# Optimization experiments

Measured on AMD Instinct MI355X. Metric: run time of the kernel, lower is better.

## Reference

```python
import jax, jax.numpy as jnp
import numpy as np

N_NODES = 100000


def gcn_conv(x, edge_index, W, b):
    """PyG GCNConv: symmetric normalization with added self-loops.
    x: [N, Fin], edge_index: [2, E], W: [Fin, Fout], b: [Fout]
    """
    n = x.shape[0]
    h = x @ W  # [N, Fout] dense transform first (standard GCNConv order)
    loops = jnp.arange(n, dtype=edge_index.dtype)
    src = jnp.concatenate([edge_index[0], loops])  # self-loops appended
    dst = jnp.concatenate([edge_index[1], loops])
    deg = jax.ops.segment_sum(jnp.ones_like(dst, dtype=h.dtype), dst, num_segments=n)
    dinv = jax.lax.rsqrt(deg)  # deg >= 1 thanks to self-loops
    norm = dinv[src] * dinv[dst]  # [E+N]
    msgs = h[src] * norm[:, None]  # gather + scale
    out = jax.ops.segment_sum(msgs, dst, num_segments=n)  # scatter-add
    return out + b


def setup_inputs() -> dict:
    key = jax.random.key(0)
    k = jax.random.split(key, 9)
    in_c, hid, out_c = 128, 128, 64
    n_edges = 1600000
    x = jax.random.normal(k[0], (N_NODES, in_c), dtype=jnp.float32)
    edge_index = jax.random.randint(k[1], (2, n_edges), 0, N_NODES, dtype=jnp.int64)
    def lin(kw, kb, fan_in, fan_out):
        bound = 1.0 / np.sqrt(fan_in)
        W = jax.random.uniform(kw, (fan_in, fan_out), jnp.float32, -bound, bound)
        b = jax.random.uniform(kb, (fan_out,), jnp.float32, -bound, bound)
        return W, b
    W1, b1 = lin(k[2], k[3], in_c, hid)
    W2, b2 = lin(k[4], k[5], hid, hid)
    Wf, bf = lin(k[6], k[7], hid, out_c)
    return {"x": x, "edge_index": edge_index, "W1": W1, "b1": b1,
            "W2": W2, "b2": b2, "Wf": Wf, "bf": bf}


def reference(x, edge_index, W1, b1, W2, b2, Wf, bf):
    h = jax.nn.relu(gcn_conv(x, edge_index, W1, b1))
    h = jax.nn.relu(gcn_conv(h, edge_index, W2, b2))
    return h @ Wf + bf
```

## Files before the change

kernel.cpp:

```cpp
#include <hip/hip_runtime.h>
#include <stdint.h>

typedef short short8 __attribute__((ext_vector_type(8)));
typedef float floatx4 __attribute__((ext_vector_type(4)));
typedef float f32x2 __attribute__((ext_vector_type(2)));

#define BK 256

static __device__ __forceinline__ float bflo(unsigned int u) {
    union { unsigned int i; float f; } v; v.i = u << 16; return v.f;
}
static __device__ __forceinline__ float bfhi(unsigned int u) {
    union { unsigned int i; float f; } v; v.i = u & 0xffff0000u; return v.f;
}
static __device__ __forceinline__ unsigned short f2bf(float f) {
    union { float f; unsigned int i; } v; v.f = f;
    unsigned int u = v.i;
    unsigned int r = u + 0x7fffu + ((u >> 16) & 1u);
    return (unsigned short)(r >> 16);
}
static __device__ __forceinline__ f32x2 unp2(unsigned int u) {
    union { unsigned int i; float f; } lo, hi;
    lo.i = u << 16; hi.i = u & 0xffff0000u;
    f32x2 r; r.x = lo.f; r.y = hi.f; return r;
}


__global__ void k_wconv_all(const float* __restrict__ W1, const float* __restrict__ W2,
                            const float* __restrict__ Wf, unsigned short* __restrict__ wb1,
                            unsigned short* __restrict__ wb2, unsigned short* __restrict__ wbf,
                            int* __restrict__ bucket_cnt) {
    int i = blockIdx.x * 256 + threadIdx.x;
    if (i < 512) bucket_cnt[i] = 0;
    if (i < 16384) {
        int k = i >> 7, n = i & 127;
        wb1[n * 128 + k] = f2bf(W1[i]);
    } else if (i < 32768) {
        int j = i - 16384, k = j >> 7, n = j & 127;
        wb2[n * 128 + k] = f2bf(W2[j]);
    } else if (i < 40960) {
        int j = i - 32768, k = j >> 6, n = j & 63;
        wbf[n * 128 + k] = f2bf(Wf[j]);
    }
}

__global__ __launch_bounds__(256) void k_hist(const int* __restrict__ dst, int* bucket_cnt,
                                              int E, int N, int K) {
    __shared__ int h[4][512];
    int t = threadIdx.x, w = t >> 6;
    for (int i = t; i < 4 * 512; i += 256) ((int*)h)[i] = 0;
    __syncthreads();
    int per = (E + gridDim.x - 1) / gridDim.x;
    int lo = blockIdx.x * per, hi = min(lo + per, E);
    for (int e = lo + t; e < hi; e += 256) {
        unsigned int d = (unsigned int)dst[e];
        if (d < (unsigned int)N) atomicAdd(&h[w][d >> 8], 1);
    }
    __syncthreads();
    for (int i = t; i < K; i += 256) {
        int c = h[0][i] + h[1][i] + h[2][i] + h[3][i];
        if (c) atomicAdd(&bucket_cnt[i], c);
    }
}

__global__ void k_scanK(const int* __restrict__ bucket_cnt, int* bucket_off, int* bucket_cur,
                        int* row_start, int K, int N) {
    __shared__ int s[512];
    int t = threadIdx.x;
    int v = (t < K) ? bucket_cnt[t] : 0;
    s[t] = v; __syncthreads();
    for (int off = 1; off < 512; off <<= 1) {
        int x = (t >= off) ? s[t - off] : 0;
        __syncthreads();
        s[t] += x;
        __syncthreads();
    }
    if (t < K) { bucket_off[t] = s[t] - v; bucket_cur[t] = s[t] - v; }
    if (t == K - 1) { bucket_off[K] = s[t]; row_start[N] = s[t]; }
}

__global__ __launch_bounds__(256) void k_binscatter(const int* __restrict__ src,
                                                    const int* __restrict__ dst,
                                                    int* bucket_cur, unsigned int* __restrict__ tmp,
                                                    int E, int N, int K) {
    __shared__ int h[4][512];
    int t = threadIdx.x, w = t >> 6;
    for (int i = t; i < 4 * 512; i += 256) ((int*)h)[i] = 0;
    __syncthreads();
    int per = (E + gridDim.x - 1) / gridDim.x;
    int lo = blockIdx.x * per, hi = min(lo + per, E);
    for (int e = lo + t; e < hi; e += 256) {
        unsigned int d = (unsigned int)dst[e];
        if (d < (unsigned int)N) atomicAdd(&h[w][d >> 8], 1);
    }
    __syncthreads();
    for (int k = t; k < K; k += 256) {
        int c0 = h[0][k], c1 = h[1][k], c2 = h[2][k], c3 = h[3][k];
        int tot = c0 + c1 + c2 + c3;
        int base = tot ? atomicAdd(&bucket_cur[k], tot) : 0;
        h[0][k] = base; h[1][k] = base + c0; h[2][k] = base + c0 + c1;
        h[3][k] = base + c0 + c1 + c2;
    }
    __syncthreads();
    for (int e = lo + t; e < hi; e += 256) {
        unsigned int d = (unsigned int)dst[e];
        if (d < (unsigned int)N) {
            unsigned int sv = (unsigned int)src[e];
            if (sv >= (unsigned int)N) sv = 0;
            int p = atomicAdd(&h[w][d >> 8], 1);
            tmp[p] = (sv << 8) | (d & 255u);
        }
    }
}

__global__ __launch_bounds__(256) void k_fine(const unsigned int* __restrict__ tmp,
                                              const int* __restrict__ bucket_off,
                                              int* __restrict__ row_start, float* __restrict__ dinv,
                                              int* __restrict__ csr, int N) {
    __shared__ int deg4[4][BK];
    __shared__ int scn[BK];
    __shared__ int cur[BK];
    int b = blockIdx.x, t = threadIdx.x, w = t >> 6;
    int lo = bucket_off[b], hi = bucket_off[b + 1];
    for (int i = t; i < 4 * BK; i += 256) ((int*)deg4)[i] = 0;
    __syncthreads();
    for (int e = lo + t; e < hi; e += 256) atomicAdd(&deg4[w][tmp[e] & 255u], 1);
    __syncthreads();
    int v = deg4[0][t] + deg4[1][t] + deg4[2][t] + deg4[3][t];
    scn[t] = v; __syncthreads();
    for (int off = 1; off < 256; off <<= 1) {
        int x = (t >= off) ? scn[t - off] : 0;
        __syncthreads();
        scn[t] += x;
        __syncthreads();
    }
    int rs = lo + scn[t] - v;
    cur[t] = rs;
    int node = b * BK + t;
    if (node < N) { row_start[node] = rs; dinv[node] = rsqrtf((float)(v + 1)); }
    __syncthreads();
    for (int e = lo + t; e < hi; e += 256) {
        unsigned int p = tmp[e];
        int pos = atomicAdd(&cur[p & 255u], 1);
        csr[pos] = (int)(p >> 8);
    }
}


template <int NOUT, bool SCALE, bool BIAS, bool XF32, bool OUTF32>
__global__ __launch_bounds__(256, 2) void k_gemm(
    const void* __restrict__ Xv, const unsigned short* __restrict__ Wbf,
    const float* __restrict__ bias, const float* __restrict__ dinv,
    void* __restrict__ outv, int M, int MB) {
    __shared__ __align__(16) unsigned short Wl[NOUT * 136];
    int t = threadIdx.x;
    for (int c = t; c < NOUT * 16; c += 256) {
        short8 v = *(const short8*)(Wbf + (size_t)c * 8);
        *(short8*)(&Wl[(c >> 4) * 136 + (c & 15) * 8]) = v;
    }
    __syncthreads();

    int wave = t >> 6, lane = t & 63;
    int quad = lane >> 4, l16 = lane & 15;
    constexpr int NT = NOUT / 16;

    for (int mb = blockIdx.x; mb < MB; mb += gridDim.x) {
        int m0 = mb * 64 + wave * 16;
        int mr = m0 + l16;
        int mrc = mr < M ? mr : M - 1;

        floatx4 acc[NT];
#pragma unroll
        for (int i = 0; i < NT; i++) acc[i] = (floatx4){0.f, 0.f, 0.f, 0.f};

#pragma unroll
        for (int kc = 0; kc < 4; kc++) {
            short8 a;
            if (XF32) {
                const float* X = (const float*)Xv;
                const float* p = X + (size_t)mrc * 128 + kc * 32 + quad * 8;
                float4 xa = *(const float4*)p;
                float4 xb = *(const float4*)(p + 4);
                a[0] = (short)f2bf(xa.x); a[1] = (short)f2bf(xa.y);
                a[2] = (short)f2bf(xa.z); a[3] = (short)f2bf(xa.w);
                a[4] = (short)f2bf(xb.x); a[5] = (short)f2bf(xb.y);
                a[6] = (short)f2bf(xb.z); a[7] = (short)f2bf(xb.w);
            } else {
                const unsigned short* X = (const unsigned short*)Xv;
                a = *(const short8*)(X + (size_t)mrc * 128 + kc * 32 + quad * 8);
            }
#pragma unroll
            for (int nt = 0; nt < NT; nt++) {
                short8 b = *(const short8*)(&Wl[(nt * 16 + l16) * 136 + kc * 32 + quad * 8]);
                acc[nt] = __builtin_amdgcn_mfma_f32_16x16x32_bf16(a, b, acc[nt], 0, 0, 0);
            }
        }

#pragma unroll
        for (int i = 0; i < 4; i++) {
            int r = m0 + quad * 4 + i;
            if (r >= M) continue;
            float sc = SCALE ? dinv[r] : 1.0f;
#pragma unroll
            for (int nt = 0; nt < NT; nt++) {
                int n = nt * 16 + l16;
                float v = acc[nt][i] * sc;
                if (BIAS) v += bias[n];
                if (OUTF32) {
                    ((float*)outv)[(size_t)r * NOUT + n] = v;
                } else {
                    ((unsigned short*)outv)[(size_t)r * NOUT + n] = f2bf(v);
                }
            }
        }
    }
}


template <int NOUT, bool SCALE, bool BIAS, bool OUTF32>
__global__ __launch_bounds__(256, 3) void k_agg_gemm(
    const unsigned short* __restrict__ Hs, const int* __restrict__ csr,
    const int* __restrict__ row_start, const float* __restrict__ dinv,
    const float* __restrict__ bias_agg, const unsigned short* __restrict__ Wbf,
    const float* __restrict__ bias_out, void* __restrict__ outv,
    int N, int E) {
    __shared__ __align__(16) unsigned short Wl[NOUT * 136];
    __shared__ __align__(16) unsigned short Xl[64 * 136];
    int t = threadIdx.x;
    for (int c = t; c < NOUT * 16; c += 256) {
        short8 v = *(const short8*)(Wbf + (size_t)c * 8);
        *(short8*)(&Wl[(c >> 4) * 136 + (c & 15) * 8]) = v;
    }

    int wave = t >> 6, lane = t & 63;
    int half = lane >> 5;
    int grp = (lane >> 4) & 1;
    int c16 = lane & 15;
    int l32 = lane & 31;
    int sbase = half << 5;
    int Nm1 = N - 1;
    unsigned int cb2 = (unsigned int)c16 << 4;
    const char* Hb = (const char*)Hs;

    float4 bA0 = *(const float4*)(bias_agg + c16 * 8);
    float4 bA1 = *(const float4*)(bias_agg + c16 * 8 + 4);

    for (int j = 0; j < 8; ++j) {
        int lr = wave * 16 + 2 * j + half;
        int node = blockIdx.x * 64 + lr;
        int node_c = node < N ? node : Nm1;

        int start = row_start[node_c];
        int end = row_start[node_c + 1];
        if (start < 0) start = 0;
        if (end > E) end = E;
        int cnt = end - start;
        if (cnt < 0) cnt = 0;

        uint4 us = *(const uint4*)(Hb + (((size_t)node_c << 8) | cb2));

        int pre = cnt < 32 ? cnt : 32;
        int idxv = 0;
        if (l32 < pre) idxv = min(max(csr[start + l32], 0), Nm1);

        f32x2 a01 = {0.f, 0.f}, a23 = {0.f, 0.f}, a45 = {0.f, 0.f}, a67 = {0.f, 0.f};
#define ACC8(u) do { a01 += unp2((u).x); a23 += unp2((u).y); \
                     a45 += unp2((u).z); a67 += unp2((u).w); } while (0)
        int full2 = pre >> 1;
        int it = 0;
        for (; it + 4 <= full2; it += 4) {
            int p = it * 2 + grp;
            int i0 = __shfl(idxv, sbase + p);
            int i1 = __shfl(idxv, sbase + p + 2);
            int i2 = __shfl(idxv, sbase + p + 4);
            int i3 = __shfl(idxv, sbase + p + 6);
            uint4 u0 = *(const uint4*)(Hb + (((unsigned int)i0 << 8) | cb2));
            uint4 u1 = *(const uint4*)(Hb + (((unsigned int)i1 << 8) | cb2));
            uint4 u2 = *(const uint4*)(Hb + (((unsigned int)i2 << 8) | cb2));
            uint4 u3 = *(const uint4*)(Hb + (((unsigned int)i3 << 8) | cb2));
            ACC8(u0); ACC8(u1); ACC8(u2); ACC8(u3);
        }
        for (; it < full2; it++) {
            int i0 = __shfl(idxv, sbase + it * 2 + grp);
            uint4 u0 = *(const uint4*)(Hb + (((unsigned int)i0 << 8) | cb2));
            ACC8(u0);
        }
        int eT = full2 * 2 + grp;
        int iT = __shfl(idxv, sbase + (eT < pre ? eT : 0));
        if (eT < pre) {
            uint4 u0 = *(const uint4*)(Hb + (((unsigned int)iT << 8) | cb2));
            ACC8(u0);
        }
        for (int e = start + 32 + grp; e < end; e += 2) {
            int ii = min(max(csr[e], 0), Nm1);
            uint4 u = *(const uint4*)(Hb + (((unsigned int)ii << 8) | cb2));
            ACC8(u);
        }
#undef ACC8

        float a0 = a01.x, a1 = a01.y, a2 = a23.x, a3 = a23.y;
        float a4 = a45.x, a5 = a45.y, a6 = a67.x, a7 = a67.y;

        a0 += __shfl_xor(a0, 16); a1 += __shfl_xor(a1, 16); a2 += __shfl_xor(a2, 16);
        a3 += __shfl_xor(a3, 16); a4 += __shfl_xor(a4, 16); a5 += __shfl_xor(a5, 16);
        a6 += __shfl_xor(a6, 16); a7 += __shfl_xor(a7, 16);

        a0 += bflo(us.x); a1 += bfhi(us.x); a2 += bflo(us.y); a3 += bfhi(us.y);
        a4 += bflo(us.z); a5 += bfhi(us.z); a6 += bflo(us.w); a7 += bfhi(us.w);

        float di = dinv[node_c];
        if (grp == 0) {
            short8 o;
            o[0] = (short)f2bf(fmaxf(fmaf(di, a0, bA0.x), 0.f));
            o[1] = (short)f2bf(fmaxf(fmaf(di, a1, bA0.y), 0.f));
            o[2] = (short)f2bf(fmaxf(fmaf(di, a2, bA0.z), 0.f));
            o[3] = (short)f2bf(fmaxf(fmaf(di, a3, bA0.w), 0.f));
            o[4] = (short)f2bf(fmaxf(fmaf(di, a4, bA1.x), 0.f));
            o[5] = (short)f2bf(fmaxf(fmaf(di, a5, bA1.y), 0.f));
            o[6] = (short)f2bf(fmaxf(fmaf(di, a6, bA1.z), 0.f));
            o[7] = (short)f2bf(fmaxf(fmaf(di, a7, bA1.w), 0.f));
            *(short8*)(&Xl[lr * 136 + c16 * 8]) = o;
        }
    }
    __syncthreads();

    int quad = lane >> 4, l16 = lane & 15;
    constexpr int NT = NOUT / 16;
    int m0 = blockIdx.x * 64 + wave * 16;

    floatx4 acc[NT];
#pragma unroll
    for (int i = 0; i < NT; i++) acc[i] = (floatx4){0.f, 0.f, 0.f, 0.f};

#pragma unroll
    for (int kc = 0; kc < 4; kc++) {
        short8 a = *(const short8*)(&Xl[(wave * 16 + l16) * 136 + kc * 32 + quad * 8]);
#pragma unroll
        for (int nt = 0; nt < NT; nt++) {
            short8 b = *(const short8*)(&Wl[(nt * 16 + l16) * 136 + kc * 32 + quad * 8]);
            acc[nt] = __builtin_amdgcn_mfma_f32_16x16x32_bf16(a, b, acc[nt], 0, 0, 0);
        }
    }

#pragma unroll
    for (int i = 0; i < 4; i++) {
        int r = m0 + quad * 4 + i;
        if (r >= N) continue;
        float sc = SCALE ? dinv[r] : 1.0f;
#pragma unroll
        for (int nt = 0; nt < NT; nt++) {
            int n = nt * 16 + l16;
            float v = acc[nt][i] * sc;
            if (BIAS) v += bias_out[n];
            if (OUTF32) {
                ((float*)outv)[(size_t)r * NOUT + n] = v;
            } else {
                ((unsigned short*)outv)[(size_t)r * NOUT + n] = f2bf(v);
            }
        }
    }
}


extern "C" void kernel_launch(void* const* d_in, const int* in_sizes, int n_in,
                              void* d_out, int out_size, void* d_ws, size_t ws_size,
                              hipStream_t stream) {
    const float* x  = (const float*)d_in[0];
    const int* ei   = (const int*)d_in[1];
    const float* W1 = (const float*)d_in[2];
    const float* b1 = (const float*)d_in[3];
    const float* W2 = (const float*)d_in[4];
    const float* b2 = (const float*)d_in[5];
    const float* Wf = (const float*)d_in[6];
    const float* bf = (const float*)d_in[7];

    int N = in_sizes[0] / 128;
    int E = in_sizes[1] / 2;
    const int* src = ei;
    const int* dst = ei + E;
    int K = (N + BK - 1) / BK;
    if (N >= (1 << 24) || K > 512) return;

    size_t need = 0;
    auto pad = [](size_t b) { return (b + 255) & ~(size_t)255; };
    size_t o_bcnt = need; need += pad(512 * 4);
    size_t o_boff = need; need += pad(513 * 4);
    size_t o_bcur = need; need += pad(512 * 4);
    size_t o_rs   = need; need += pad(((size_t)N + 1) * 4);
    size_t o_dinv = need; need += pad((size_t)N * 4);
    size_t o_wbf  = need; need += pad((16384 + 16384 + 8192) * 2);
    size_t o_csr  = need; need += pad((size_t)E * 4);
    size_t o_hs   = need; need += pad((size_t)N * 128 * 2);
    size_t o_a    = need; need += pad((size_t)N * 128 * 2);
    if (ws_size < need) return;
    if ((size_t)E * 4 > (size_t)N * 128 * 2) return;

    char* ws = (char*)d_ws;
    int* bucket_cnt = (int*)(ws + o_bcnt);
    int* bucket_off = (int*)(ws + o_boff);
    int* bucket_cur = (int*)(ws + o_bcur);
    int* row_start  = (int*)(ws + o_rs);
    float* dinv     = (float*)(ws + o_dinv);
    unsigned short* wb1 = (unsigned short*)(ws + o_wbf);
    unsigned short* wb2 = wb1 + 16384;
    unsigned short* wbf = wb2 + 16384;
    int* csr        = (int*)(ws + o_csr);
    unsigned short* Hs  = (unsigned short*)(ws + o_hs);
    unsigned short* Hs2 = (unsigned short*)(ws + o_a);
    unsigned int* tmp   = (unsigned int*)Hs2;

    k_wconv_all<<<160, 256, 0, stream>>>(W1, W2, Wf, wb1, wb2, wbf, bucket_cnt);
    k_hist<<<256, 256, 0, stream>>>(dst, bucket_cnt, E, N, K);
    k_scanK<<<1, 512, 0, stream>>>(bucket_cnt, bucket_off, bucket_cur, row_start, K, N);
    k_binscatter<<<256, 256, 0, stream>>>(src, dst, bucket_cur, tmp, E, N, K);
    k_fine<<<K, 256, 0, stream>>>(tmp, bucket_off, row_start, dinv, csr, N);

    int MB = (N + 63) / 64;
    int GG = (MB + 1) / 2;

    k_gemm<128, true, false, true, false><<<GG, 256, 0, stream>>>(x, wb1, nullptr, dinv, Hs, N, MB);
    k_agg_gemm<128, true, false, false><<<MB, 256, 0, stream>>>(
        Hs, csr, row_start, dinv, b1, wb2, nullptr, Hs2, N, E);
    k_agg_gemm<64, false, true, true><<<MB, 256, 0, stream>>>(
        Hs2, csr, row_start, dinv, b2, wbf, bf, d_out, N, E);
}
```

Baseline: 348.6 us.

## Fuse bucket scan into histogram kernel and drop LDS weight staging in agg_gemm

The single-block scan kernel is folded into the histogram kernel: the last block to finish, detected with an atomic counter and a threadfence, scans the 512 bucket counts and writes the offsets. This removes one kernel launch. In the aggregation+GEMM kernel the weight matrix is no longer staged in shared memory. B fragments are read directly from global memory (L2/L1 cached), the output columns are processed in 64-wide halves to cut accumulator registers, and launch bounds rise from 3 to 8 blocks per SM. This trades redundant global loads of weights for lower LDS use and higher occupancy in the gather-heavy aggregation.

```diff
diff --git a/kernel.cpp b/kernel.cpp
--- a/kernel.cpp
+++ b/kernel.cpp
@@ -29,8 +29,9 @@
 __global__ void k_wconv_all(const float* __restrict__ W1, const float* __restrict__ W2,
                             const float* __restrict__ Wf, unsigned short* __restrict__ wb1,
                             unsigned short* __restrict__ wb2, unsigned short* __restrict__ wbf,
-                            int* __restrict__ bucket_cnt) {
+                            int* __restrict__ bucket_cnt, int* __restrict__ done) {
     int i = blockIdx.x * 256 + threadIdx.x;
+    if (i == 0) *done = 0;
     if (i < 512) bucket_cnt[i] = 0;
     if (i < 16384) {
         int k = i >> 7, n = i & 127;
@@ -44,9 +45,12 @@
     }
 }
 
-__global__ __launch_bounds__(256) void k_hist(const int* __restrict__ dst, int* bucket_cnt,
-                                              int E, int N, int K) {
+__global__ __launch_bounds__(256) void k_hist_scan(
+    const int* __restrict__ dst, int* bucket_cnt, int* bucket_off, int* bucket_cur,
+    int* __restrict__ row_start, int* __restrict__ done, int E, int N, int K) {
     __shared__ int h[4][512];
+    __shared__ int s[256];
+    __shared__ int isLast;
     int t = threadIdx.x, w = t >> 6;
     for (int i = t; i < 4 * 512; i += 256) ((int*)h)[i] = 0;
     __syncthreads();
@@ -61,22 +65,25 @@
         int c = h[0][i] + h[1][i] + h[2][i] + h[3][i];
         if (c) atomicAdd(&bucket_cnt[i], c);
     }
-}
-
-__global__ void k_scanK(const int* __restrict__ bucket_cnt, int* bucket_off, int* bucket_cur,
-                        int* row_start, int K, int N) {
-    __shared__ int s[512];
-    int t = threadIdx.x;
-    int v = (t < K) ? bucket_cnt[t] : 0;
-    s[t] = v; __syncthreads();
-    for (int off = 1; off < 512; off <<= 1) {
+    __threadfence();
+    __syncthreads();
+    if (t == 0) isLast = (atomicAdd(done, 1) == (int)gridDim.x - 1);
+    __syncthreads();
+    if (!isLast) return;
+    int e0 = atomicAdd(&bucket_cnt[2 * t], 0);
+    int e1 = atomicAdd(&bucket_cnt[2 * t + 1], 0);
+    int p = e0 + e1;
+    s[t] = p; __syncthreads();
+    for (int off = 1; off < 256; off <<= 1) {
         int x = (t >= off) ? s[t - off] : 0;
         __syncthreads();
         s[t] += x;
         __syncthreads();
     }
-    if (t < K) { bucket_off[t] = s[t] - v; bucket_cur[t] = s[t] - v; }
-    if (t == K - 1) { bucket_off[K] = s[t]; row_start[N] = s[t]; }
+    int incl = s[t], excl = incl - p;
+    bucket_off[2 * t] = excl;          bucket_cur[2 * t] = excl;
+    bucket_off[2 * t + 1] = excl + e0; bucket_cur[2 * t + 1] = excl + e0;
+    if (t == 255) { bucket_off[512] = incl; row_start[N] = incl; }
 }
 
 __global__ __launch_bounds__(256) void k_binscatter(const int* __restrict__ src,
@@ -218,20 +225,14 @@
 
 
 template <int NOUT, bool SCALE, bool BIAS, bool OUTF32>
-__global__ __launch_bounds__(256, 3) void k_agg_gemm(
+__global__ __launch_bounds__(256, 8) void k_agg_gemm(
     const unsigned short* __restrict__ Hs, const int* __restrict__ csr,
     const int* __restrict__ row_start, const float* __restrict__ dinv,
     const float* __restrict__ bias_agg, const unsigned short* __restrict__ Wbf,
     const float* __restrict__ bias_out, void* __restrict__ outv,
     int N, int E) {
-    __shared__ __align__(16) unsigned short Wl[NOUT * 136];
     __shared__ __align__(16) unsigned short Xl[64 * 136];
     int t = threadIdx.x;
-    for (int c = t; c < NOUT * 16; c += 256) {
-        short8 v = *(const short8*)(Wbf + (size_t)c * 8);
-        *(short8*)(&Wl[(c >> 4) * 136 + (c & 15) * 8]) = v;
-    }
-
     int wave = t >> 6, lane = t & 63;
     int half = lane >> 5;
     int grp = (lane >> 4) & 1;
@@ -325,37 +326,41 @@
     __syncthreads();
 
     int quad = lane >> 4, l16 = lane & 15;
-    constexpr int NT = NOUT / 16;
+    constexpr int NH = NOUT / 64;
     int m0 = blockIdx.x * 64 + wave * 16;
 
-    floatx4 acc[NT];
-#pragma unroll
-    for (int i = 0; i < NT; i++) acc[i] = (floatx4){0.f, 0.f, 0.f, 0.f};
-
-#pragma unroll
-    for (int kc = 0; kc < 4; kc++) {
-        short8 a = *(const short8*)(&Xl[(wave * 16 + l16) * 136 + kc * 32 + quad * 8]);
-#pragma unroll
-        for (int nt = 0; nt < NT; nt++) {
-            short8 b = *(const short8*)(&Wl[(nt * 16 + l16) * 136 + kc * 32 + quad * 8]);
-            acc[nt] = __builtin_amdgcn_mfma_f32_16x16x32_bf16(a, b, acc[nt], 0, 0, 0);
-        }
-    }
-
-#pragma unroll
-    for (int i = 0; i < 4; i++) {
-        int r = m0 + quad * 4 + i;
-        if (r >= N) continue;
-        float sc = SCALE ? dinv[r] : 1.0f;
-#pragma unroll
-        for (int nt = 0; nt < NT; nt++) {
-            int n = nt * 16 + l16;
-            float v = acc[nt][i] * sc;
-            if (BIAS) v += bias_out[n];
-            if (OUTF32) {
-                ((float*)outv)[(size_t)r * NOUT + n] = v;
-            } else {
-                ((unsigned short*)outv)[(size_t)r * NOUT + n] = f2bf(v);
+#pragma unroll
+    for (int hh = 0; hh < NH; hh++) {
+        floatx4 acc[4];
+#pragma unroll
+        for (int i = 0; i < 4; i++) acc[i] = (floatx4){0.f, 0.f, 0.f, 0.f};
+
+#pragma unroll
+        for (int kc = 0; kc < 4; kc++) {
+            short8 a = *(const short8*)(&Xl[(wave * 16 + l16) * 136 + kc * 32 + quad * 8]);
+#pragma unroll
+            for (int nt = 0; nt < 4; nt++) {
+                int n = hh * 64 + nt * 16 + l16;
+                short8 b = *(const short8*)(Wbf + (size_t)n * 128 + kc * 32 + quad * 8);
+                acc[nt] = __builtin_amdgcn_mfma_f32_16x16x32_bf16(a, b, acc[nt], 0, 0, 0);
+            }
+        }
+
+#pragma unroll
+        for (int i = 0; i < 4; i++) {
+            int r = m0 + quad * 4 + i;
+            if (r >= N) continue;
+            float sc = SCALE ? dinv[r] : 1.0f;
+#pragma unroll
+            for (int nt = 0; nt < 4; nt++) {
+                int n = hh * 64 + nt * 16 + l16;
+                float v = acc[nt][i] * sc;
+                if (BIAS) v += bias_out[n];
+                if (OUTF32) {
+                    ((float*)outv)[(size_t)r * NOUT + n] = v;
+                } else {
+                    ((unsigned short*)outv)[(size_t)r * NOUT + n] = f2bf(v);
+                }
             }
         }
     }
@@ -386,6 +391,7 @@
     size_t o_bcnt = need; need += pad(512 * 4);
     size_t o_boff = need; need += pad(513 * 4);
     size_t o_bcur = need; need += pad(512 * 4);
+    size_t o_flag = need; need += pad(4);
     size_t o_rs   = need; need += pad(((size_t)N + 1) * 4);
     size_t o_dinv = need; need += pad((size_t)N * 4);
     size_t o_wbf  = need; need += pad((16384 + 16384 + 8192) * 2);
@@ -399,6 +405,7 @@
     int* bucket_cnt = (int*)(ws + o_bcnt);
     int* bucket_off = (int*)(ws + o_boff);
     int* bucket_cur = (int*)(ws + o_bcur);
+    int* done       = (int*)(ws + o_flag);
     int* row_start  = (int*)(ws + o_rs);
     float* dinv     = (float*)(ws + o_dinv);
     unsigned short* wb1 = (unsigned short*)(ws + o_wbf);
@@ -409,9 +416,9 @@
     unsigned short* Hs2 = (unsigned short*)(ws + o_a);
     unsigned int* tmp   = (unsigned int*)Hs2;
 
-    k_wconv_all<<<160, 256, 0, stream>>>(W1, W2, Wf, wb1, wb2, wbf, bucket_cnt);
-    k_hist<<<256, 256, 0, stream>>>(dst, bucket_cnt, E, N, K);
-    k_scanK<<<1, 512, 0, stream>>>(bucket_cnt, bucket_off, bucket_cur, row_start, K, N);
+    k_wconv_all<<<160, 256, 0, stream>>>(W1, W2, Wf, wb1, wb2, wbf, bucket_cnt, done);
+    k_hist_scan<<<256, 256, 0, stream>>>(dst, bucket_cnt, bucket_off, bucket_cur,
+                                         row_start, done, E, N, K);
     k_binscatter<<<256, 256, 0, stream>>>(src, dst, bucket_cur, tmp, E, N, K);
     k_fine<<<K, 256, 0, stream>>>(tmp, bucket_off, row_start, dinv, csr, N);
 
```

Result: no change. 345.8 us (-0.8%).
